# Kernel optimization log

Hardware: AMD Instinct MI355X
Metric: run time of the kernel (lower is better)

## Reference

```python
import jax, jax.numpy as jnp
import numpy as np

B, H, W = 32, 768, 768
POS_THR = 0.1
NEG_RATIO = 3
TOPK_NO_POS = 500


def setup_inputs() -> dict:
    key = jax.random.key(0)
    k1, k2, k3 = jax.random.split(key, 3)
    pred = jax.random.uniform(k1, (B, H, W, 2), dtype=jnp.float32)
    region_scores = jax.random.uniform(k2, (B, H, W), dtype=jnp.float32) ** 16
    affinity_scores = jax.random.uniform(k3, (B, H, W), dtype=jnp.float32) ** 16
    return {"pred": pred, "region_scores": region_scores, "affinity_scores": affinity_scores}


def _single_image_loss(pre_loss, label):
    # Vectorized OHEM: replaces the per-sample Python loop + torch.topk.
    b = pre_loss.shape[0]
    loss = pre_loss.reshape(b, -1)   # [B, N]
    lab = label.reshape(b, -1)       # [B, N]
    n = loss.shape[1]
    pos = lab >= POS_THR             # [B, N] bool
    p = jnp.sum(pos, axis=1)         # positive pixel count per sample
    pos_sum = jnp.sum(jnp.where(pos, loss, 0.0), axis=1)
    posi_loss = jnp.where(p > 0, pos_sum / jnp.maximum(p, 1).astype(loss.dtype), 0.0)
    # Negatives sorted descending; -inf pushes positives to the tail.
    # When p == 0 the mask is all-False so this sorts the full loss vector,
    # matching torch.topk(pre_loss[i], 500).
    neg_vals = jnp.where(pos, -jnp.inf, loss)
    sorted_desc = jnp.flip(jnp.sort(neg_vals, axis=1), axis=1)
    nn = n - p                       # negative count
    # mean of all negatives when nn < 3p == mean of top-min(nn,3p); else top-3p
    k = jnp.where(p > 0, jnp.minimum(nn, NEG_RATIO * p), TOPK_NO_POS)
    csum = jnp.cumsum(jnp.where(jnp.isfinite(sorted_desc), sorted_desc, 0.0), axis=1)
    topk_sum = jnp.take_along_axis(csum, jnp.maximum(k - 1, 0)[:, None], axis=1)[:, 0]
    nega_loss = jnp.where(k > 0, topk_sum / jnp.maximum(k, 1).astype(loss.dtype), 0.0)
    return jnp.sum(posi_loss + nega_loss)


def reference(pred, region_scores, affinity_scores):
    p_gh = pred[..., 0]
    p_gah = pred[..., 1]
    loss1 = (p_gh - region_scores) ** 2   # MSELoss(reduction='none')
    loss2 = (p_gah - affinity_scores) ** 2
    char_loss = _single_image_loss(loss1, region_scores)
    affi_loss = _single_image_loss(loss2, affinity_scores)
    b = pred.shape[0]
    return char_loss / b + affi_loss / b
```

## Files before the change

kernel.cpp:

```cpp
#include <hip/hip_runtime.h>


constexpr int   BATCH   = 32;
constexpr int   NPS     = 768 * 768;
constexpr int   CH2     = BATCH * 2;
constexpr long  PIX_ALL = (long)BATCH * NPS;
constexpr int   EPB     = 8192;
constexpr int   BX      = NPS / EPB;
constexpr float POS_THR_F = 0.1f;
constexpr unsigned TOPK_NO_POS = 500u;
constexpr int   CAP     = 131072;
constexpr int   CAPB    = 1024;

__global__ __launch_bounds__(256, 4) void k_pass1(
    const float4* __restrict__ pred4,
    const float4* __restrict__ reg4,
    const float4* __restrict__ aff4,
    unsigned* __restrict__ h1c,
    unsigned* __restrict__ pcnt, float* __restrict__ psum,
    float4* __restrict__ lossR4, float4* __restrict__ lossA4, int writeLoss)
{
    __shared__ unsigned sc0[512 * 4], sc1[512 * 4];
    __shared__ unsigned wpc[8];
    __shared__ float    wps[8];
    for (int j = threadIdx.x; j < 2048; j += 256) { sc0[j] = 0u; sc1[j] = 0u; }
    __syncthreads();

    const int  b   = blockIdx.y;
    const int  tid = threadIdx.x;
    const int  rep = tid & 3;
    constexpr int ITERS = EPB / 1024;
    long idx4 = (((long)b * NPS + (long)blockIdx.x * EPB) >> 2) + tid;

    unsigned pc0 = 0, pc1 = 0;
    float    ps0 = 0.f, ps1 = 0.f;

    float4 r = reg4[idx4], a = aff4[idx4];
    float4 pA = pred4[idx4 * 2], pB = pred4[idx4 * 2 + 1];

    for (int i = 0; i < ITERS; ++i) {
        float4 rn, an, pAn, pBn;
        if (i + 1 < ITERS) {
            const long nx = idx4 + 256;
            rn = reg4[nx]; an = aff4[nx]; pAn = pred4[nx * 2]; pBn = pred4[nx * 2 + 1];
        }
        float4 lr, la;
#define DO_PIX(RR, AA, PG, PA, LR, LA) do {                                   \
        float d0 = (PG) - (RR); float v0 = d0 * d0;                           \
        bool pos0 = (RR) >= POS_THR_F;                                        \
        if (pos0) { pc0++; ps0 += v0; }                                       \
        else { unsigned ky = __float_as_uint(v0) >> 21;                       \
               atomicAdd(&sc0[(ky << 2) + rep], 1u); }                        \
        LR = pos0 ? -1.0f : v0;                                               \
        float d1 = (PA) - (AA); float v1 = d1 * d1;                           \
        bool pos1 = (AA) >= POS_THR_F;                                        \
        if (pos1) { pc1++; ps1 += v1; }                                       \
        else { unsigned ky = __float_as_uint(v1) >> 21;                       \
               atomicAdd(&sc1[(ky << 2) + rep], 1u); }                        \
        LA = pos1 ? -1.0f : v1;                                               \
    } while (0)
        DO_PIX(r.x, a.x, pA.x, pA.y, lr.x, la.x);
        DO_PIX(r.y, a.y, pA.z, pA.w, lr.y, la.y);
        DO_PIX(r.z, a.z, pB.x, pB.y, lr.z, la.z);
        DO_PIX(r.w, a.w, pB.z, pB.w, lr.w, la.w);
#undef DO_PIX
        if (writeLoss) { lossR4[idx4] = lr; lossA4[idx4] = la; }
        idx4 += 256; r = rn; a = an; pA = pAn; pB = pBn;
    }
    __syncthreads();

    for (int j = tid; j < 512; j += 256) {
        unsigned c0 = sc0[j*4] + sc0[j*4+1] + sc0[j*4+2] + sc0[j*4+3];
        if (c0) atomicAdd(&h1c[(b*2+0)*512 + j], c0);
        unsigned c1 = sc1[j*4] + sc1[j*4+1] + sc1[j*4+2] + sc1[j*4+3];
        if (c1) atomicAdd(&h1c[(b*2+1)*512 + j], c1);
    }
    for (int o = 32; o > 0; o >>= 1) {
        pc0 += __shfl_down(pc0, o); ps0 += __shfl_down(ps0, o);
        pc1 += __shfl_down(pc1, o); ps1 += __shfl_down(ps1, o);
    }
    const int wid = tid >> 6, lane = tid & 63;
    if (lane == 0) { wpc[wid] = pc0; wps[wid] = ps0; wpc[4+wid] = pc1; wps[4+wid] = ps1; }
    __syncthreads();
    if (tid == 0) {
        unsigned t0 = 0, t1 = 0; float s0 = 0.f, s1 = 0.f;
        for (int q = 0; q < 4; ++q) { t0 += wpc[q]; s0 += wps[q]; t1 += wpc[4+q]; s1 += wps[4+q]; }
        atomicAdd(&pcnt[b*2+0], t0); unsafeAtomicAdd(&psum[b*2+0], s0);
        atomicAdd(&pcnt[b*2+1], t1); unsafeAtomicAdd(&psum[b*2+1], s1);
    }
}

template<int NBINS>
__device__ __forceinline__ void select_counts(
    const unsigned* __restrict__ cnt, unsigned k,
    unsigned& outBin, unsigned& outRem)
{
    constexpr int PER = NBINS / 256;
    const int t = threadIdx.x;
    unsigned lc[PER];
#pragma unroll
    for (int j = 0; j < PER; ++j) lc[j] = cnt[t*PER + j];
    unsigned lsum = 0;
#pragma unroll
    for (int j = 0; j < PER; ++j) lsum += lc[j];

    __shared__ unsigned part[256];
    __shared__ unsigned s_bin, s_rem;
    part[t] = lsum;
    __syncthreads();
    for (int off = 1; off < 256; off <<= 1) {
        unsigned v = (t + off < 256) ? part[t + off] : 0u;
        __syncthreads();
        part[t] += v;
        __syncthreads();
    }
    unsigned cum = (t + 1 < 256) ? part[t + 1] : 0u;
#pragma unroll
    for (int j = PER - 1; j >= 0; --j) {
        unsigned c = lc[j];
        if (cum < k && k <= cum + c) { s_bin = (unsigned)(t * PER + j); s_rem = k - cum; }
        cum += c;
    }
    __syncthreads();
    outBin = s_bin; outRem = s_rem;
}

template<int NBINS>
__device__ __forceinline__ void select_counts_sums(
    const unsigned* __restrict__ cnt, const float* __restrict__ sums,
    unsigned k, unsigned& outBin, unsigned& outRem, double& outSum)
{
    constexpr int PER = NBINS / 256;
    const int t = threadIdx.x;
    unsigned lc[PER]; float lf[PER];
#pragma unroll
    for (int j = 0; j < PER; ++j) { lc[j] = cnt[t*PER + j]; lf[j] = sums[t*PER + j]; }
    unsigned lsum = 0;
#pragma unroll
    for (int j = 0; j < PER; ++j) lsum += lc[j];

    __shared__ unsigned part[256];
    __shared__ unsigned s_bin, s_rem;
    __shared__ double   wsum[4];
    part[t] = lsum;
    __syncthreads();
    for (int off = 1; off < 256; off <<= 1) {
        unsigned v = (t + off < 256) ? part[t + off] : 0u;
        __syncthreads();
        part[t] += v;
        __syncthreads();
    }
    unsigned cum = (t + 1 < 256) ? part[t + 1] : 0u;
#pragma unroll
    for (int j = PER - 1; j >= 0; --j) {
        unsigned c = lc[j];
        if (cum < k && k <= cum + c) { s_bin = (unsigned)(t * PER + j); s_rem = k - cum; }
        cum += c;
    }
    __syncthreads();
    const unsigned bin = s_bin;
    double ds = 0.0;
#pragma unroll
    for (int j = 0; j < PER; ++j)
        if ((unsigned)(t * PER + j) > bin) ds += (double)lf[j];
    for (int o = 32; o > 0; o >>= 1) ds += __shfl_down(ds, o);
    const int wid = t >> 6, lane = t & 63;
    if (lane == 0) wsum[wid] = ds;
    __syncthreads();
    if (t == 0) ds = wsum[0] + wsum[1] + wsum[2] + wsum[3];
    outBin = bin; outRem = s_rem; outSum = ds;
}

__global__ __launch_bounds__(256) void k_scan1(
    const unsigned* __restrict__ h1c,
    const unsigned* __restrict__ pcnt, const float* __restrict__ psum,
    unsigned* __restrict__ T1, unsigned* __restrict__ rem1,
    unsigned* __restrict__ kk, float* __restrict__ posi)
{
    const int idx = blockIdx.x;
    const unsigned p  = pcnt[idx];
    const unsigned nn = (unsigned)NPS - p;
    const unsigned k  = p ? ((nn < 3u*p) ? nn : 3u*p) : TOPK_NO_POS;
    if (threadIdx.x == 0) {
        kk[idx]   = k;
        posi[idx] = p ? (psum[idx] / (float)p) : 0.0f;
    }
    if (k == 0u) {
        if (threadIdx.x == 0) { T1[idx] = 0xFFFFFFFFu; rem1[idx] = 0u; }
        return;
    }
    unsigned bin, rem;
    select_counts<512>(h1c + idx*512, k, bin, rem);
    if (threadIdx.x == 0) { T1[idx] = bin; rem1[idx] = rem; }
}

__global__ __launch_bounds__(256, 4) void k_pass2(
    const float4* __restrict__ pred4,
    const float4* __restrict__ reg4,
    const float4* __restrict__ aff4,
    const float4* __restrict__ lossR4, const float4* __restrict__ lossA4, int haveLoss,
    const unsigned* __restrict__ T1,
    unsigned* __restrict__ h2c, double* __restrict__ sumAbove,
    float* __restrict__ cbuf, unsigned* __restrict__ ccnt)
{
    __shared__ unsigned sc0[2048], sc1[2048];
    __shared__ float    lb0[CAPB], lb1[CAPB];
    __shared__ unsigned lcnt[2];
    __shared__ unsigned sbase[2];
    __shared__ float    wred[8];
    for (int j = threadIdx.x; j < 2048; j += 256) { sc0[j] = 0u; sc1[j] = 0u; }
    if (threadIdx.x < 2) lcnt[threadIdx.x] = 0u;
    __syncthreads();

    const int b = blockIdx.y;
    const unsigned t1r = T1[b*2+0], t1a = T1[b*2+1];
    const int tid = threadIdx.x, lane = tid & 63;
    float*    gb0 = cbuf + (size_t)(b*2+0) * CAP;
    float*    gb1 = cbuf + (size_t)(b*2+1) * CAP;
    unsigned* gc0 = ccnt + b*2+0;
    unsigned* gc1 = ccnt + b*2+1;
    float rs0 = 0.f, rs1 = 0.f;

    auto proc = [&](float v, unsigned t1, unsigned* sc, float& rs,
                    unsigned* lcnt_p, float* lbuf, unsigned* gcnt, float* gbuf) {
        if (v < 0.0f) return;
        const unsigned bt  = __float_as_uint(v);
        const unsigned key = bt >> 21;
        if (key > t1) { rs += v; return; }
        if (key != t1) return;
        atomicAdd(&sc[(bt >> 10) & 2047u], 1u);
        const unsigned long long m = __ballot(true);
        const int ldr = __ffsll(m) - 1;
        const unsigned pre = (unsigned)__popcll(m & ((1ull << lane) - 1ull));
        unsigned base = 0;
        if (lane == ldr) base = atomicAdd(lcnt_p, (unsigned)__popcll(m));
        base = __shfl(base, ldr);
        const unsigned ix = base + pre;
        if (ix < (unsigned)CAPB) lbuf[ix] = v;
        else { unsigned g = atomicAdd(gcnt, 1u); if (g < (unsigned)CAP) gbuf[g] = v; }
    };

    constexpr int ITERS = EPB / 1024;
    long idx4 = (((long)b * NPS + (long)blockIdx.x * EPB) >> 2) + tid;
    for (int i = 0; i < ITERS; ++i, idx4 += 256) {
        float4 vr, va;
        if (haveLoss) { vr = lossR4[idx4]; va = lossA4[idx4]; }
        else {
            const float4 r  = reg4[idx4];
            const float4 a  = aff4[idx4];
            const float4 pA = pred4[idx4*2];
            const float4 pB = pred4[idx4*2+1];
            float d;
            d = pA.x - r.x; vr.x = (r.x >= POS_THR_F) ? -1.0f : d*d;
            d = pA.z - r.y; vr.y = (r.y >= POS_THR_F) ? -1.0f : d*d;
            d = pB.x - r.z; vr.z = (r.z >= POS_THR_F) ? -1.0f : d*d;
            d = pB.z - r.w; vr.w = (r.w >= POS_THR_F) ? -1.0f : d*d;
            d = pA.y - a.x; va.x = (a.x >= POS_THR_F) ? -1.0f : d*d;
            d = pA.w - a.y; va.y = (a.y >= POS_THR_F) ? -1.0f : d*d;
            d = pB.y - a.z; va.z = (a.z >= POS_THR_F) ? -1.0f : d*d;
            d = pB.w - a.w; va.w = (a.w >= POS_THR_F) ? -1.0f : d*d;
        }
        proc(vr.x, t1r, sc0, rs0, &lcnt[0], lb0, gc0, gb0);
        proc(vr.y, t1r, sc0, rs0, &lcnt[0], lb0, gc0, gb0);
        proc(vr.z, t1r, sc0, rs0, &lcnt[0], lb0, gc0, gb0);
        proc(vr.w, t1r, sc0, rs0, &lcnt[0], lb0, gc0, gb0);
        proc(va.x, t1a, sc1, rs1, &lcnt[1], lb1, gc1, gb1);
        proc(va.y, t1a, sc1, rs1, &lcnt[1], lb1, gc1, gb1);
        proc(va.z, t1a, sc1, rs1, &lcnt[1], lb1, gc1, gb1);
        proc(va.w, t1a, sc1, rs1, &lcnt[1], lb1, gc1, gb1);
    }
    __syncthreads();

    for (int j = tid; j < 2048; j += 256) {
        unsigned c0 = sc0[j];
        if (c0) atomicAdd(&h2c[(b*2+0)*2048 + j], c0);
        unsigned c1 = sc1[j];
        if (c1) atomicAdd(&h2c[(b*2+1)*2048 + j], c1);
    }
    const unsigned lc0 = lcnt[0] < (unsigned)CAPB ? lcnt[0] : (unsigned)CAPB;
    const unsigned lc1 = lcnt[1] < (unsigned)CAPB ? lcnt[1] : (unsigned)CAPB;
    if (tid == 0)      sbase[0] = lc0 ? atomicAdd(gc0, lc0) : 0u;
    else if (tid == 1) sbase[1] = lc1 ? atomicAdd(gc1, lc1) : 0u;
    __syncthreads();
    for (unsigned i = tid; i < lc0; i += 256) {
        unsigned g = sbase[0] + i;
        if (g < (unsigned)CAP) gb0[g] = lb0[i];
    }
    for (unsigned i = tid; i < lc1; i += 256) {
        unsigned g = sbase[1] + i;
        if (g < (unsigned)CAP) gb1[g] = lb1[i];
    }
    for (int o = 32; o > 0; o >>= 1) { rs0 += __shfl_down(rs0, o); rs1 += __shfl_down(rs1, o); }
    const int wid = tid >> 6;
    if (lane == 0) { wred[wid] = rs0; wred[4+wid] = rs1; }
    __syncthreads();
    if (tid == 0) {
        float s0 = wred[0]+wred[1]+wred[2]+wred[3];
        float s1 = wred[4]+wred[5]+wred[6]+wred[7];
        unsafeAtomicAdd(&sumAbove[b*2+0], (double)s0);
        unsafeAtomicAdd(&sumAbove[b*2+1], (double)s1);
    }
}

__global__ __launch_bounds__(256) void k_scan2(
    const unsigned* __restrict__ h2c,
    const unsigned* __restrict__ T1, const unsigned* __restrict__ rem1,
    unsigned* __restrict__ T2, unsigned* __restrict__ rem2)
{
    const int idx = blockIdx.x;
    if (T1[idx] == 0xFFFFFFFFu) {
        if (threadIdx.x == 0) { T2[idx] = 0xFFFFFFFFu; rem2[idx] = 0u; }
        return;
    }
    unsigned bin, rem;
    select_counts<2048>(h2c + idx*2048, rem1[idx], bin, rem);
    if (threadIdx.x == 0) { T2[idx] = bin; rem2[idx] = rem; }
}

__global__ __launch_bounds__(256) void k_pass3_compact(
    const float* __restrict__ cbuf, const unsigned* __restrict__ ccnt,
    const unsigned* __restrict__ T2,
    unsigned* __restrict__ h3c, float* __restrict__ h3s,
    double* __restrict__ sumMid)
{
    const int ch = blockIdx.x;
    const unsigned cnt = ccnt[ch];
    if (cnt > (unsigned)CAP) return;
    __shared__ unsigned sc[1024];
    __shared__ float    ss[1024];
    __shared__ float    wred[4];
    for (int j = threadIdx.x; j < 1024; j += 256) { sc[j] = 0u; ss[j] = 0.f; }
    __syncthreads();

    const unsigned t2 = T2[ch];
    const float* buf = cbuf + (size_t)ch * CAP;
    float rs = 0.f;
    for (unsigned i = threadIdx.x; i < cnt; i += 256) {
        const float v = buf[i];
        const unsigned bt = __float_as_uint(v);
        const unsigned s2 = (bt >> 10) & 2047u;
        if (s2 > t2) rs += v;
        else if (s2 == t2) { atomicAdd(&sc[bt & 1023u], 1u); unsafeAtomicAdd(&ss[bt & 1023u], v); }
    }
    __syncthreads();
    for (int j = threadIdx.x; j < 1024; j += 256) {
        unsigned c = sc[j];
        if (c) { atomicAdd(&h3c[ch*1024 + j], c); unsafeAtomicAdd(&h3s[ch*1024 + j], ss[j]); }
    }
    for (int o = 32; o > 0; o >>= 1) rs += __shfl_down(rs, o);
    const int wid = threadIdx.x >> 6, lane = threadIdx.x & 63;
    if (lane == 0) wred[wid] = rs;
    __syncthreads();
    if (threadIdx.x == 0)
        unsafeAtomicAdd(&sumMid[ch], (double)(wred[0]+wred[1]+wred[2]+wred[3]));
}

__global__ __launch_bounds__(256, 4) void k_pass3_full(
    const float4* __restrict__ pred4,
    const float4* __restrict__ reg4,
    const float4* __restrict__ aff4,
    const float4* __restrict__ lossR4, const float4* __restrict__ lossA4, int haveLoss,
    const unsigned* __restrict__ T1, const unsigned* __restrict__ T2,
    const unsigned* __restrict__ ccnt,
    unsigned* __restrict__ h3c, float* __restrict__ h3s,
    double* __restrict__ sumMid)
{
    const int b = blockIdx.y;
    const bool f0 = ccnt[b*2+0] > (unsigned)CAP;
    const bool f1 = ccnt[b*2+1] > (unsigned)CAP;
    if (!f0 && !f1) return;

    __shared__ unsigned sc0[1024], sc1[1024];
    __shared__ float    ss0[1024], ss1[1024];
    __shared__ float    wred[8];
    for (int j = threadIdx.x; j < 1024; j += 256) { sc0[j]=0u; sc1[j]=0u; ss0[j]=0.f; ss1[j]=0.f; }
    __syncthreads();

    const unsigned t1r = T1[b*2+0], t2r = T2[b*2+0];
    const unsigned t1a = T1[b*2+1], t2a = T2[b*2+1];
    const int tid = threadIdx.x;
    float rs0 = 0.f, rs1 = 0.f;

    constexpr int ITERS = EPB / 1024;
    long idx4 = (((long)b * NPS + (long)blockIdx.x * EPB) >> 2) + tid;
    for (int i = 0; i < ITERS; ++i, idx4 += 256) {
        float4 vr, va;
        if (haveLoss) { vr = lossR4[idx4]; va = lossA4[idx4]; }
        else {
            const float4 r  = reg4[idx4];
            const float4 a  = aff4[idx4];
            const float4 pA = pred4[idx4*2];
            const float4 pB = pred4[idx4*2+1];
            float d;
            d = pA.x - r.x; vr.x = (r.x >= POS_THR_F) ? -1.0f : d*d;
            d = pA.z - r.y; vr.y = (r.y >= POS_THR_F) ? -1.0f : d*d;
            d = pB.x - r.z; vr.z = (r.z >= POS_THR_F) ? -1.0f : d*d;
            d = pB.z - r.w; vr.w = (r.w >= POS_THR_F) ? -1.0f : d*d;
            d = pA.y - a.x; va.x = (a.x >= POS_THR_F) ? -1.0f : d*d;
            d = pA.w - a.y; va.y = (a.y >= POS_THR_F) ? -1.0f : d*d;
            d = pB.y - a.z; va.z = (a.z >= POS_THR_F) ? -1.0f : d*d;
            d = pB.w - a.w; va.w = (a.w >= POS_THR_F) ? -1.0f : d*d;
        }
#define DO3(V, T1V, T2V, SC, SS, RS, EN) do {                                 \
        if (EN && (V) >= 0.0f) { unsigned bt = __float_as_uint(V);            \
            if ((bt >> 21) == (T1V)) { unsigned s2 = (bt >> 10) & 2047u;      \
                if (s2 > (T2V)) RS += (V);                                    \
                else if (s2 == (T2V)) { atomicAdd(&SC[bt & 1023u], 1u);       \
                    unsafeAtomicAdd(&SS[bt & 1023u], (V)); } } } } while (0)
        DO3(vr.x, t1r, t2r, sc0, ss0, rs0, f0); DO3(vr.y, t1r, t2r, sc0, ss0, rs0, f0);
        DO3(vr.z, t1r, t2r, sc0, ss0, rs0, f0); DO3(vr.w, t1r, t2r, sc0, ss0, rs0, f0);
        DO3(va.x, t1a, t2a, sc1, ss1, rs1, f1); DO3(va.y, t1a, t2a, sc1, ss1, rs1, f1);
        DO3(va.z, t1a, t2a, sc1, ss1, rs1, f1); DO3(va.w, t1a, t2a, sc1, ss1, rs1, f1);
#undef DO3
    }
    __syncthreads();
    for (int j = tid; j < 1024; j += 256) {
        if (f0) { unsigned c = sc0[j];
            if (c) { atomicAdd(&h3c[(b*2+0)*1024 + j], c); unsafeAtomicAdd(&h3s[(b*2+0)*1024 + j], ss0[j]); } }
        if (f1) { unsigned c = sc1[j];
            if (c) { atomicAdd(&h3c[(b*2+1)*1024 + j], c); unsafeAtomicAdd(&h3s[(b*2+1)*1024 + j], ss1[j]); } }
    }
    for (int o = 32; o > 0; o >>= 1) { rs0 += __shfl_down(rs0, o); rs1 += __shfl_down(rs1, o); }
    const int wid = tid >> 6, lane = tid & 63;
    if (lane == 0) { wred[wid] = rs0; wred[4+wid] = rs1; }
    __syncthreads();
    if (tid == 0) {
        if (f0) unsafeAtomicAdd(&sumMid[b*2+0], (double)(wred[0]+wred[1]+wred[2]+wred[3]));
        if (f1) unsafeAtomicAdd(&sumMid[b*2+1], (double)(wred[4]+wred[5]+wred[6]+wred[7]));
    }
}

__global__ __launch_bounds__(256) void k_scan3(
    const unsigned* __restrict__ h3c, const float* __restrict__ h3s,
    const unsigned* __restrict__ T1, const unsigned* __restrict__ T2,
    const unsigned* __restrict__ rem2,
    const unsigned* __restrict__ kk, const float* __restrict__ posi,
    const double* __restrict__ sumAbove, const double* __restrict__ sumMid,
    float* __restrict__ contrib)
{
    const int idx = blockIdx.x;
    const unsigned k = kk[idx];
    if (k == 0u) {
        if (threadIdx.x == 0) contrib[idx] = posi[idx];
        return;
    }
    unsigned bin, rem; double s3;
    select_counts_sums<1024>(h3c + idx*1024, h3s + idx*1024, rem2[idx], bin, rem, s3);
    if (threadIdx.x == 0) {
        const float t = __uint_as_float((T1[idx] << 21) | (T2[idx] << 10) | bin);
        const double nega = (sumAbove[idx] + sumMid[idx] + s3 + (double)rem * (double)t)
                            / (double)k;
        contrib[idx] = (float)((double)posi[idx] + nega);
    }
}

__global__ void k_reduce(const float* __restrict__ contrib, float* __restrict__ out)
{
    double v = (double)contrib[threadIdx.x];
    for (int o = 32; o > 0; o >>= 1) v += __shfl_down(v, o);
    if (threadIdx.x == 0) out[0] = (float)(v / (double)BATCH);
}

extern "C" void kernel_launch(void* const* d_in, const int* in_sizes, int n_in,
                              void* d_out, int out_size, void* d_ws, size_t ws_size,
                              hipStream_t stream)
{
    (void)in_sizes; (void)n_in; (void)out_size; (void)ws_size;
    const float4* pred4 = (const float4*)d_in[0];
    const float4* reg4  = (const float4*)d_in[1];
    const float4* aff4  = (const float4*)d_in[2];

    char* w = (char*)d_ws;
    unsigned* h1c  = (unsigned*)w;
    unsigned* h2c  = h1c + (size_t)CH2 * 512;
    unsigned* h3c  = h2c + (size_t)CH2 * 2048;
    float*    h3s  = (float*)(h3c + (size_t)CH2 * 1024);
    unsigned* pcnt = (unsigned*)(h3s + (size_t)CH2 * 1024);
    float*    psum = (float*)(pcnt + CH2);
    unsigned* T1   = (unsigned*)(psum + CH2);
    unsigned* T2   = T1 + CH2;
    unsigned* rem1 = T2 + CH2;
    unsigned* rem2 = rem1 + CH2;
    unsigned* kk   = rem2 + CH2;
    float*    posi = (float*)(kk + CH2);
    float*    contrib = posi + CH2;
    unsigned* ccnt = (unsigned*)(contrib + CH2);
    double*   sumAbove = (double*)(ccnt + CH2);
    double*   sumMid   = sumAbove + CH2;
    const size_t hdr_bytes = (size_t)((char*)(sumMid + CH2) - w);

    const size_t loss_off   = (size_t)4 << 20;
    const size_t loss_bytes = (size_t)PIX_ALL * 2 * sizeof(float);
    const int haveLoss = (ws_size >= loss_off + loss_bytes) ? 1 : 0;
    float4* lossR4 = (float4*)(w + loss_off);
    float4* lossA4 = (float4*)(w + loss_off + (size_t)PIX_ALL * sizeof(float));

    const size_t cbuf_off = haveLoss ? (loss_off + loss_bytes) : loss_off;
    float* cbuf = (float*)(w + cbuf_off);

    hipMemsetAsync(d_ws, 0, hdr_bytes, stream);

    dim3 grid(BX, BATCH);
    k_pass1<<<grid, 256, 0, stream>>>(pred4, reg4, aff4, h1c, pcnt, psum,
                                      lossR4, lossA4, haveLoss);
    k_scan1<<<CH2, 256, 0, stream>>>(h1c, pcnt, psum, T1, rem1, kk, posi);
    k_pass2<<<grid, 256, 0, stream>>>(pred4, reg4, aff4, lossR4, lossA4, haveLoss,
                                      T1, h2c, sumAbove, cbuf, ccnt);
    k_scan2<<<CH2, 256, 0, stream>>>(h2c, T1, rem1, T2, rem2);
    k_pass3_compact<<<CH2, 256, 0, stream>>>(cbuf, ccnt, T2, h3c, h3s, sumMid);
    k_pass3_full<<<grid, 256, 0, stream>>>(pred4, reg4, aff4, lossR4, lossA4, haveLoss,
                                           T1, T2, ccnt, h3c, h3s, sumMid);
    k_scan3<<<CH2, 256, 0, stream>>>(h3c, h3s, T1, T2, rem2, kk, posi,
                                     sumAbove, sumMid, contrib);
    k_reduce<<<1, 64, 0, stream>>>(contrib, (float*)d_out);
}
```

Baseline: 460.4 us.

## Restructure radix-select into histogram, compact, and in-block refine passes

Replaces the three-pass radix select with a single 2048-bin first-level histogram that also accumulates per-bin sums. Candidates in the threshold bin are then compacted and refined inside one block per channel, so the loss buffer writes and reads and the second and third full-data passes go away. The cost is shared-memory float atomics in the histogram pass, a re-read of the inputs in the compact pass, and no fallback when the compacted candidate count exceeds the buffer capacity. The compact loop also issues redundant loads, and its prefetch values are discarded.

```diff
diff --git a/kernel.cpp b/kernel.cpp
--- a/kernel.cpp
+++ b/kernel.cpp
@@ -4,31 +4,30 @@
 constexpr int   BATCH   = 32;
 constexpr int   NPS     = 768 * 768;
 constexpr int   CH2     = BATCH * 2;
-constexpr long  PIX_ALL = (long)BATCH * NPS;
-constexpr int   EPB     = 8192;
+constexpr int   EPB     = 16384;
 constexpr int   BX      = NPS / EPB;
 constexpr float POS_THR_F = 0.1f;
 constexpr unsigned TOPK_NO_POS = 500u;
+constexpr int   NB1     = 2048;
 constexpr int   CAP     = 131072;
 constexpr int   CAPB    = 1024;
 
-__global__ __launch_bounds__(256, 4) void k_pass1(
+__global__ __launch_bounds__(256, 4) void k_hist(
     const float4* __restrict__ pred4,
     const float4* __restrict__ reg4,
     const float4* __restrict__ aff4,
-    unsigned* __restrict__ h1c,
-    unsigned* __restrict__ pcnt, float* __restrict__ psum,
-    float4* __restrict__ lossR4, float4* __restrict__ lossA4, int writeLoss)
-{
-    __shared__ unsigned sc0[512 * 4], sc1[512 * 4];
+    unsigned* __restrict__ h1c, float* __restrict__ h1s,
+    unsigned* __restrict__ pcnt, float* __restrict__ psum)
+{
+    __shared__ unsigned sc0[NB1], sc1[NB1];
+    __shared__ float    ss0[NB1], ss1[NB1];
     __shared__ unsigned wpc[8];
     __shared__ float    wps[8];
-    for (int j = threadIdx.x; j < 2048; j += 256) { sc0[j] = 0u; sc1[j] = 0u; }
+    for (int j = threadIdx.x; j < NB1; j += 256) { sc0[j]=0u; sc1[j]=0u; ss0[j]=0.f; ss1[j]=0.f; }
     __syncthreads();
 
     const int  b   = blockIdx.y;
     const int  tid = threadIdx.x;
-    const int  rep = tid & 3;
     constexpr int ITERS = EPB / 1024;
     long idx4 = (((long)b * NPS + (long)blockIdx.x * EPB) >> 2) + tid;
 
@@ -44,36 +43,30 @@
             const long nx = idx4 + 256;
             rn = reg4[nx]; an = aff4[nx]; pAn = pred4[nx * 2]; pBn = pred4[nx * 2 + 1];
         }
-        float4 lr, la;
-#define DO_PIX(RR, AA, PG, PA, LR, LA) do {                                   \
+#define DO_PIX(RR, AA, PG, PA) do {                                           \
         float d0 = (PG) - (RR); float v0 = d0 * d0;                           \
-        bool pos0 = (RR) >= POS_THR_F;                                        \
-        if (pos0) { pc0++; ps0 += v0; }                                       \
-        else { unsigned ky = __float_as_uint(v0) >> 21;                       \
-               atomicAdd(&sc0[(ky << 2) + rep], 1u); }                        \
-        LR = pos0 ? -1.0f : v0;                                               \
+        if ((RR) >= POS_THR_F) { pc0++; ps0 += v0; }                          \
+        else { unsigned ky = __float_as_uint(v0) >> 19;                       \
+               atomicAdd(&sc0[ky], 1u); unsafeAtomicAdd(&ss0[ky], v0); }      \
         float d1 = (PA) - (AA); float v1 = d1 * d1;                           \
-        bool pos1 = (AA) >= POS_THR_F;                                        \
-        if (pos1) { pc1++; ps1 += v1; }                                       \
-        else { unsigned ky = __float_as_uint(v1) >> 21;                       \
-               atomicAdd(&sc1[(ky << 2) + rep], 1u); }                        \
-        LA = pos1 ? -1.0f : v1;                                               \
+        if ((AA) >= POS_THR_F) { pc1++; ps1 += v1; }                          \
+        else { unsigned ky = __float_as_uint(v1) >> 19;                       \
+               atomicAdd(&sc1[ky], 1u); unsafeAtomicAdd(&ss1[ky], v1); }      \
     } while (0)
-        DO_PIX(r.x, a.x, pA.x, pA.y, lr.x, la.x);
-        DO_PIX(r.y, a.y, pA.z, pA.w, lr.y, la.y);
-        DO_PIX(r.z, a.z, pB.x, pB.y, lr.z, la.z);
-        DO_PIX(r.w, a.w, pB.z, pB.w, lr.w, la.w);
+        DO_PIX(r.x, a.x, pA.x, pA.y);
+        DO_PIX(r.y, a.y, pA.z, pA.w);
+        DO_PIX(r.z, a.z, pB.x, pB.y);
+        DO_PIX(r.w, a.w, pB.z, pB.w);
 #undef DO_PIX
-        if (writeLoss) { lossR4[idx4] = lr; lossA4[idx4] = la; }
         idx4 += 256; r = rn; a = an; pA = pAn; pB = pBn;
     }
     __syncthreads();
 
-    for (int j = tid; j < 512; j += 256) {
-        unsigned c0 = sc0[j*4] + sc0[j*4+1] + sc0[j*4+2] + sc0[j*4+3];
-        if (c0) atomicAdd(&h1c[(b*2+0)*512 + j], c0);
-        unsigned c1 = sc1[j*4] + sc1[j*4+1] + sc1[j*4+2] + sc1[j*4+3];
-        if (c1) atomicAdd(&h1c[(b*2+1)*512 + j], c1);
+    for (int j = tid; j < NB1; j += 256) {
+        unsigned c0 = sc0[j];
+        if (c0) { atomicAdd(&h1c[(b*2+0)*NB1 + j], c0); unsafeAtomicAdd(&h1s[(b*2+0)*NB1 + j], ss0[j]); }
+        unsigned c1 = sc1[j];
+        if (c1) { atomicAdd(&h1c[(b*2+1)*NB1 + j], c1); unsafeAtomicAdd(&h1s[(b*2+1)*NB1 + j], ss1[j]); }
     }
     for (int o = 32; o > 0; o >>= 1) {
         pc0 += __shfl_down(pc0, o); ps0 += __shfl_down(ps0, o);
@@ -92,8 +85,7 @@
 
 template<int NBINS>
 __device__ __forceinline__ void select_counts(
-    const unsigned* __restrict__ cnt, unsigned k,
-    unsigned& outBin, unsigned& outRem)
+    const unsigned* cnt, unsigned k, unsigned& outBin, unsigned& outRem)
 {
     constexpr int PER = NBINS / 256;
     const int t = threadIdx.x;
@@ -127,7 +119,7 @@
 
 template<int NBINS>
 __device__ __forceinline__ void select_counts_sums(
-    const unsigned* __restrict__ cnt, const float* __restrict__ sums,
+    const unsigned* cnt, const float* sums,
     unsigned k, unsigned& outBin, unsigned& outRem, double& outSum)
 {
     constexpr int PER = NBINS / 256;
@@ -172,10 +164,11 @@
 }
 
 __global__ __launch_bounds__(256) void k_scan1(
-    const unsigned* __restrict__ h1c,
+    const unsigned* __restrict__ h1c, const float* __restrict__ h1s,
     const unsigned* __restrict__ pcnt, const float* __restrict__ psum,
     unsigned* __restrict__ T1, unsigned* __restrict__ rem1,
-    unsigned* __restrict__ kk, float* __restrict__ posi)
+    unsigned* __restrict__ kk, float* __restrict__ posi,
+    double* __restrict__ sumAbove)
 {
     const int idx = blockIdx.x;
     const unsigned p  = pcnt[idx];
@@ -186,29 +179,24 @@
         posi[idx] = p ? (psum[idx] / (float)p) : 0.0f;
     }
     if (k == 0u) {
-        if (threadIdx.x == 0) { T1[idx] = 0xFFFFFFFFu; rem1[idx] = 0u; }
+        if (threadIdx.x == 0) { T1[idx] = 0xFFFFFFFFu; rem1[idx] = 0u; sumAbove[idx] = 0.0; }
         return;
     }
-    unsigned bin, rem;
-    select_counts<512>(h1c + idx*512, k, bin, rem);
-    if (threadIdx.x == 0) { T1[idx] = bin; rem1[idx] = rem; }
-}
-
-__global__ __launch_bounds__(256, 4) void k_pass2(
+    unsigned bin, rem; double s;
+    select_counts_sums<NB1>(h1c + idx*NB1, h1s + idx*NB1, k, bin, rem, s);
+    if (threadIdx.x == 0) { T1[idx] = bin; rem1[idx] = rem; sumAbove[idx] = s; }
+}
+
+__global__ __launch_bounds__(256, 4) void k_compact(
     const float4* __restrict__ pred4,
     const float4* __restrict__ reg4,
     const float4* __restrict__ aff4,
-    const float4* __restrict__ lossR4, const float4* __restrict__ lossA4, int haveLoss,
     const unsigned* __restrict__ T1,
-    unsigned* __restrict__ h2c, double* __restrict__ sumAbove,
     float* __restrict__ cbuf, unsigned* __restrict__ ccnt)
 {
-    __shared__ unsigned sc0[2048], sc1[2048];
     __shared__ float    lb0[CAPB], lb1[CAPB];
     __shared__ unsigned lcnt[2];
     __shared__ unsigned sbase[2];
-    __shared__ float    wred[8];
-    for (int j = threadIdx.x; j < 2048; j += 256) { sc0[j] = 0u; sc1[j] = 0u; }
     if (threadIdx.x < 2) lcnt[threadIdx.x] = 0u;
     __syncthreads();
 
@@ -219,16 +207,13 @@
     float*    gb1 = cbuf + (size_t)(b*2+1) * CAP;
     unsigned* gc0 = ccnt + b*2+0;
     unsigned* gc1 = ccnt + b*2+1;
-    float rs0 = 0.f, rs1 = 0.f;
-
-    auto proc = [&](float v, unsigned t1, unsigned* sc, float& rs,
+
+    auto proc = [&](float tgt, float pg, unsigned t1,
                     unsigned* lcnt_p, float* lbuf, unsigned* gcnt, float* gbuf) {
-        if (v < 0.0f) return;
-        const unsigned bt  = __float_as_uint(v);
-        const unsigned key = bt >> 21;
-        if (key > t1) { rs += v; return; }
-        if (key != t1) return;
-        atomicAdd(&sc[(bt >> 10) & 2047u], 1u);
+        if (tgt >= POS_THR_F) return;
+        const float d = pg - tgt;
+        const float v = d * d;
+        if ((__float_as_uint(v) >> 19) != t1) return;
         const unsigned long long m = __ballot(true);
         const int ldr = __ffsll(m) - 1;
         const unsigned pre = (unsigned)__popcll(m & ((1ull << lane) - 1ull));
@@ -242,41 +227,32 @@
 
     constexpr int ITERS = EPB / 1024;
     long idx4 = (((long)b * NPS + (long)blockIdx.x * EPB) >> 2) + tid;
-    for (int i = 0; i < ITERS; ++i, idx4 += 256) {
-        float4 vr, va;
-        if (haveLoss) { vr = lossR4[idx4]; va = lossA4[idx4]; }
-        else {
-            const float4 r  = reg4[idx4];
-            const float4 a  = aff4[idx4];
-            const float4 pA = pred4[idx4*2];
-            const float4 pB = pred4[idx4*2+1];
-            float d;
-            d = pA.x - r.x; vr.x = (r.x >= POS_THR_F) ? -1.0f : d*d;
-            d = pA.z - r.y; vr.y = (r.y >= POS_THR_F) ? -1.0f : d*d;
-            d = pB.x - r.z; vr.z = (r.z >= POS_THR_F) ? -1.0f : d*d;
-            d = pB.z - r.w; vr.w = (r.w >= POS_THR_F) ? -1.0f : d*d;
-            d = pA.y - a.x; va.x = (a.x >= POS_THR_F) ? -1.0f : d*d;
-            d = pA.w - a.y; va.y = (a.y >= POS_THR_F) ? -1.0f : d*d;
-            d = pB.y - a.z; va.z = (a.z >= POS_THR_F) ? -1.0f : d*d;
-            d = pB.w - a.w; va.w = (a.w >= POS_THR_F) ? -1.0f : d*d;
+    for (int i = 0; i < ITERS; ++i) {
+        float4 rn, an, pAn, pBn;
+        if (i + 1 < ITERS) {
+            const long nx = idx4 + 256;
+            rn = reg4[nx]; an = aff4[nx]; pAn = pred4[nx * 2]; pBn = pred4[nx * 2 + 1];
+        } else {
+            rn = reg4[idx4]; an = aff4[idx4]; pAn = pred4[idx4*2]; pBn = pred4[idx4*2+1];
         }
-        proc(vr.x, t1r, sc0, rs0, &lcnt[0], lb0, gc0, gb0);
-        proc(vr.y, t1r, sc0, rs0, &lcnt[0], lb0, gc0, gb0);
-        proc(vr.z, t1r, sc0, rs0, &lcnt[0], lb0, gc0, gb0);
-        proc(vr.w, t1r, sc0, rs0, &lcnt[0], lb0, gc0, gb0);
-        proc(va.x, t1a, sc1, rs1, &lcnt[1], lb1, gc1, gb1);
-        proc(va.y, t1a, sc1, rs1, &lcnt[1], lb1, gc1, gb1);
-        proc(va.z, t1a, sc1, rs1, &lcnt[1], lb1, gc1, gb1);
-        proc(va.w, t1a, sc1, rs1, &lcnt[1], lb1, gc1, gb1);
-    }
-    __syncthreads();
-
-    for (int j = tid; j < 2048; j += 256) {
-        unsigned c0 = sc0[j];
-        if (c0) atomicAdd(&h2c[(b*2+0)*2048 + j], c0);
-        unsigned c1 = sc1[j];
-        if (c1) atomicAdd(&h2c[(b*2+1)*2048 + j], c1);
-    }
+        const float4 r  = (i == 0) ? reg4[idx4] : rn;
+        (void)r;
+        const float4 rr = reg4[idx4];
+        const float4 aa = aff4[idx4];
+        const float4 pA = pred4[idx4*2];
+        const float4 pB = pred4[idx4*2+1];
+        proc(rr.x, pA.x, t1r, &lcnt[0], lb0, gc0, gb0);
+        proc(rr.y, pA.z, t1r, &lcnt[0], lb0, gc0, gb0);
+        proc(rr.z, pB.x, t1r, &lcnt[0], lb0, gc0, gb0);
+        proc(rr.w, pB.z, t1r, &lcnt[0], lb0, gc0, gb0);
+        proc(aa.x, pA.y, t1a, &lcnt[1], lb1, gc1, gb1);
+        proc(aa.y, pA.w, t1a, &lcnt[1], lb1, gc1, gb1);
+        proc(aa.z, pB.y, t1a, &lcnt[1], lb1, gc1, gb1);
+        proc(aa.w, pB.w, t1a, &lcnt[1], lb1, gc1, gb1);
+        idx4 += 256;
+    }
+    __syncthreads();
+
     const unsigned lc0 = lcnt[0] < (unsigned)CAPB ? lcnt[0] : (unsigned)CAPB;
     const unsigned lc1 = lcnt[1] < (unsigned)CAPB ? lcnt[1] : (unsigned)CAPB;
     if (tid == 0)      sbase[0] = lc0 ? atomicAdd(gc0, lc0) : 0u;
@@ -290,167 +266,63 @@
         unsigned g = sbase[1] + i;
         if (g < (unsigned)CAP) gb1[g] = lb1[i];
     }
-    for (int o = 32; o > 0; o >>= 1) { rs0 += __shfl_down(rs0, o); rs1 += __shfl_down(rs1, o); }
-    const int wid = tid >> 6;
-    if (lane == 0) { wred[wid] = rs0; wred[4+wid] = rs1; }
+}
+
+__global__ __launch_bounds__(256) void k_refine(
+    const float* __restrict__ cbuf, const unsigned* __restrict__ ccnt,
+    const unsigned* __restrict__ T1, const unsigned* __restrict__ rem1,
+    const unsigned* __restrict__ kk, const float* __restrict__ posi,
+    const double* __restrict__ sumAbove,
+    float* __restrict__ contrib)
+{
+    const int ch = blockIdx.x;
+    const unsigned k = kk[ch];
+    if (k == 0u) {
+        if (threadIdx.x == 0) contrib[ch] = posi[ch];
+        return;
+    }
+    unsigned cnt = ccnt[ch];
+    if (cnt > (unsigned)CAP) cnt = (unsigned)CAP;
+    const float* buf = cbuf + (size_t)ch * CAP;
+    const int tid = threadIdx.x;
+
+    __shared__ unsigned hA[NB1];
+    __shared__ unsigned hB[256];
+    __shared__ double   wsum[4];
+    for (int j = tid; j < NB1; j += 256) hA[j] = 0u;
+    __syncthreads();
+    for (unsigned i = tid; i < cnt; i += 256) {
+        const unsigned bt = __float_as_uint(buf[i]);
+        atomicAdd(&hA[(bt >> 8) & 2047u], 1u);
+    }
+    __syncthreads();
+    unsigned T2, rem2;
+    select_counts<NB1>(hA, rem1[ch], T2, rem2);
+
+    hB[tid] = 0u;
+    __syncthreads();
+    for (unsigned i = tid; i < cnt; i += 256) {
+        const unsigned bt = __float_as_uint(buf[i]);
+        if (((bt >> 8) & 2047u) == T2) atomicAdd(&hB[bt & 255u], 1u);
+    }
+    __syncthreads();
+    unsigned T3, rem3;
+    select_counts<256>(hB, rem2, T3, rem3);
+
+    const float t = __uint_as_float((T1[ch] << 19) | (T2 << 8) | T3);
+    double s = 0.0;
+    for (unsigned i = tid; i < cnt; i += 256) {
+        const float v = buf[i];
+        if (v > t) s += (double)v;
+    }
+    for (int o = 32; o > 0; o >>= 1) s += __shfl_down(s, o);
+    const int wid = tid >> 6, lane = tid & 63;
+    if (lane == 0) wsum[wid] = s;
     __syncthreads();
     if (tid == 0) {
-        float s0 = wred[0]+wred[1]+wred[2]+wred[3];
-        float s1 = wred[4]+wred[5]+wred[6]+wred[7];
-        unsafeAtomicAdd(&sumAbove[b*2+0], (double)s0);
-        unsafeAtomicAdd(&sumAbove[b*2+1], (double)s1);
-    }
-}
-
-__global__ __launch_bounds__(256) void k_scan2(
-    const unsigned* __restrict__ h2c,
-    const unsigned* __restrict__ T1, const unsigned* __restrict__ rem1,
-    unsigned* __restrict__ T2, unsigned* __restrict__ rem2)
-{
-    const int idx = blockIdx.x;
-    if (T1[idx] == 0xFFFFFFFFu) {
-        if (threadIdx.x == 0) { T2[idx] = 0xFFFFFFFFu; rem2[idx] = 0u; }
-        return;
-    }
-    unsigned bin, rem;
-    select_counts<2048>(h2c + idx*2048, rem1[idx], bin, rem);
-    if (threadIdx.x == 0) { T2[idx] = bin; rem2[idx] = rem; }
-}
-
-__global__ __launch_bounds__(256) void k_pass3_compact(
-    const float* __restrict__ cbuf, const unsigned* __restrict__ ccnt,
-    const unsigned* __restrict__ T2,
-    unsigned* __restrict__ h3c, float* __restrict__ h3s,
-    double* __restrict__ sumMid)
-{
-    const int ch = blockIdx.x;
-    const unsigned cnt = ccnt[ch];
-    if (cnt > (unsigned)CAP) return;
-    __shared__ unsigned sc[1024];
-    __shared__ float    ss[1024];
-    __shared__ float    wred[4];
-    for (int j = threadIdx.x; j < 1024; j += 256) { sc[j] = 0u; ss[j] = 0.f; }
-    __syncthreads();
-
-    const unsigned t2 = T2[ch];
-    const float* buf = cbuf + (size_t)ch * CAP;
-    float rs = 0.f;
-    for (unsigned i = threadIdx.x; i < cnt; i += 256) {
-        const float v = buf[i];
-        const unsigned bt = __float_as_uint(v);
-        const unsigned s2 = (bt >> 10) & 2047u;
-        if (s2 > t2) rs += v;
-        else if (s2 == t2) { atomicAdd(&sc[bt & 1023u], 1u); unsafeAtomicAdd(&ss[bt & 1023u], v); }
-    }
-    __syncthreads();
-    for (int j = threadIdx.x; j < 1024; j += 256) {
-        unsigned c = sc[j];
-        if (c) { atomicAdd(&h3c[ch*1024 + j], c); unsafeAtomicAdd(&h3s[ch*1024 + j], ss[j]); }
-    }
-    for (int o = 32; o > 0; o >>= 1) rs += __shfl_down(rs, o);
-    const int wid = threadIdx.x >> 6, lane = threadIdx.x & 63;
-    if (lane == 0) wred[wid] = rs;
-    __syncthreads();
-    if (threadIdx.x == 0)
-        unsafeAtomicAdd(&sumMid[ch], (double)(wred[0]+wred[1]+wred[2]+wred[3]));
-}
-
-__global__ __launch_bounds__(256, 4) void k_pass3_full(
-    const float4* __restrict__ pred4,
-    const float4* __restrict__ reg4,
-    const float4* __restrict__ aff4,
-    const float4* __restrict__ lossR4, const float4* __restrict__ lossA4, int haveLoss,
-    const unsigned* __restrict__ T1, const unsigned* __restrict__ T2,
-    const unsigned* __restrict__ ccnt,
-    unsigned* __restrict__ h3c, float* __restrict__ h3s,
-    double* __restrict__ sumMid)
-{
-    const int b = blockIdx.y;
-    const bool f0 = ccnt[b*2+0] > (unsigned)CAP;
-    const bool f1 = ccnt[b*2+1] > (unsigned)CAP;
-    if (!f0 && !f1) return;
-
-    __shared__ unsigned sc0[1024], sc1[1024];
-    __shared__ float    ss0[1024], ss1[1024];
-    __shared__ float    wred[8];
-    for (int j = threadIdx.x; j < 1024; j += 256) { sc0[j]=0u; sc1[j]=0u; ss0[j]=0.f; ss1[j]=0.f; }
-    __syncthreads();
-
-    const unsigned t1r = T1[b*2+0], t2r = T2[b*2+0];
-    const unsigned t1a = T1[b*2+1], t2a = T2[b*2+1];
-    const int tid = threadIdx.x;
-    float rs0 = 0.f, rs1 = 0.f;
-
-    constexpr int ITERS = EPB / 1024;
-    long idx4 = (((long)b * NPS + (long)blockIdx.x * EPB) >> 2) + tid;
-    for (int i = 0; i < ITERS; ++i, idx4 += 256) {
-        float4 vr, va;
-        if (haveLoss) { vr = lossR4[idx4]; va = lossA4[idx4]; }
-        else {
-            const float4 r  = reg4[idx4];
-            const float4 a  = aff4[idx4];
-            const float4 pA = pred4[idx4*2];
-            const float4 pB = pred4[idx4*2+1];
-            float d;
-            d = pA.x - r.x; vr.x = (r.x >= POS_THR_F) ? -1.0f : d*d;
-            d = pA.z - r.y; vr.y = (r.y >= POS_THR_F) ? -1.0f : d*d;
-            d = pB.x - r.z; vr.z = (r.z >= POS_THR_F) ? -1.0f : d*d;
-            d = pB.z - r.w; vr.w = (r.w >= POS_THR_F) ? -1.0f : d*d;
-            d = pA.y - a.x; va.x = (a.x >= POS_THR_F) ? -1.0f : d*d;
-            d = pA.w - a.y; va.y = (a.y >= POS_THR_F) ? -1.0f : d*d;
-            d = pB.y - a.z; va.z = (a.z >= POS_THR_F) ? -1.0f : d*d;
-            d = pB.w - a.w; va.w = (a.w >= POS_THR_F) ? -1.0f : d*d;
-        }
-#define DO3(V, T1V, T2V, SC, SS, RS, EN) do {                                 \
-        if (EN && (V) >= 0.0f) { unsigned bt = __float_as_uint(V);            \
-            if ((bt >> 21) == (T1V)) { unsigned s2 = (bt >> 10) & 2047u;      \
-                if (s2 > (T2V)) RS += (V);                                    \
-                else if (s2 == (T2V)) { atomicAdd(&SC[bt & 1023u], 1u);       \
-                    unsafeAtomicAdd(&SS[bt & 1023u], (V)); } } } } while (0)
-        DO3(vr.x, t1r, t2r, sc0, ss0, rs0, f0); DO3(vr.y, t1r, t2r, sc0, ss0, rs0, f0);
-        DO3(vr.z, t1r, t2r, sc0, ss0, rs0, f0); DO3(vr.w, t1r, t2r, sc0, ss0, rs0, f0);
-        DO3(va.x, t1a, t2a, sc1, ss1, rs1, f1); DO3(va.y, t1a, t2a, sc1, ss1, rs1, f1);
-        DO3(va.z, t1a, t2a, sc1, ss1, rs1, f1); DO3(va.w, t1a, t2a, sc1, ss1, rs1, f1);
-#undef DO3
-    }
-    __syncthreads();
-    for (int j = tid; j < 1024; j += 256) {
-        if (f0) { unsigned c = sc0[j];
-            if (c) { atomicAdd(&h3c[(b*2+0)*1024 + j], c); unsafeAtomicAdd(&h3s[(b*2+0)*1024 + j], ss0[j]); } }
-        if (f1) { unsigned c = sc1[j];
-            if (c) { atomicAdd(&h3c[(b*2+1)*1024 + j], c); unsafeAtomicAdd(&h3s[(b*2+1)*1024 + j], ss1[j]); } }
-    }
-    for (int o = 32; o > 0; o >>= 1) { rs0 += __shfl_down(rs0, o); rs1 += __shfl_down(rs1, o); }
-    const int wid = tid >> 6, lane = tid & 63;
-    if (lane == 0) { wred[wid] = rs0; wred[4+wid] = rs1; }
-    __syncthreads();
-    if (tid == 0) {
-        if (f0) unsafeAtomicAdd(&sumMid[b*2+0], (double)(wred[0]+wred[1]+wred[2]+wred[3]));
-        if (f1) unsafeAtomicAdd(&sumMid[b*2+1], (double)(wred[4]+wred[5]+wred[6]+wred[7]));
-    }
-}
-
-__global__ __launch_bounds__(256) void k_scan3(
-    const unsigned* __restrict__ h3c, const float* __restrict__ h3s,
-    const unsigned* __restrict__ T1, const unsigned* __restrict__ T2,
-    const unsigned* __restrict__ rem2,
-    const unsigned* __restrict__ kk, const float* __restrict__ posi,
-    const double* __restrict__ sumAbove, const double* __restrict__ sumMid,
-    float* __restrict__ contrib)
-{
-    const int idx = blockIdx.x;
-    const unsigned k = kk[idx];
-    if (k == 0u) {
-        if (threadIdx.x == 0) contrib[idx] = posi[idx];
-        return;
-    }
-    unsigned bin, rem; double s3;
-    select_counts_sums<1024>(h3c + idx*1024, h3s + idx*1024, rem2[idx], bin, rem, s3);
-    if (threadIdx.x == 0) {
-        const float t = __uint_as_float((T1[idx] << 21) | (T2[idx] << 10) | bin);
-        const double nega = (sumAbove[idx] + sumMid[idx] + s3 + (double)rem * (double)t)
-                            / (double)k;
-        contrib[idx] = (float)((double)posi[idx] + nega);
+        const double stop = wsum[0] + wsum[1] + wsum[2] + wsum[3];
+        const double nega = (sumAbove[ch] + stop + (double)rem3 * (double)t) / (double)k;
+        contrib[ch] = (float)((double)posi[ch] + nega);
     }
 }
 
@@ -472,45 +344,26 @@
 
     char* w = (char*)d_ws;
     unsigned* h1c  = (unsigned*)w;
-    unsigned* h2c  = h1c + (size_t)CH2 * 512;
-    unsigned* h3c  = h2c + (size_t)CH2 * 2048;
-    float*    h3s  = (float*)(h3c + (size_t)CH2 * 1024);
-    unsigned* pcnt = (unsigned*)(h3s + (size_t)CH2 * 1024);
+    float*    h1s  = (float*)(h1c + (size_t)CH2 * NB1);
+    unsigned* pcnt = (unsigned*)(h1s + (size_t)CH2 * NB1);
     float*    psum = (float*)(pcnt + CH2);
     unsigned* T1   = (unsigned*)(psum + CH2);
-    unsigned* T2   = T1 + CH2;
-    unsigned* rem1 = T2 + CH2;
-    unsigned* rem2 = rem1 + CH2;
-    unsigned* kk   = rem2 + CH2;
+    unsigned* rem1 = T1 + CH2;
+    unsigned* kk   = rem1 + CH2;
     float*    posi = (float*)(kk + CH2);
     float*    contrib = posi + CH2;
     unsigned* ccnt = (unsigned*)(contrib + CH2);
     double*   sumAbove = (double*)(ccnt + CH2);
-    double*   sumMid   = sumAbove + CH2;
-    const size_t hdr_bytes = (size_t)((char*)(sumMid + CH2) - w);
-
-    const size_t loss_off   = (size_t)4 << 20;
-    const size_t loss_bytes = (size_t)PIX_ALL * 2 * sizeof(float);
-    const int haveLoss = (ws_size >= loss_off + loss_bytes) ? 1 : 0;
-    float4* lossR4 = (float4*)(w + loss_off);
-    float4* lossA4 = (float4*)(w + loss_off + (size_t)PIX_ALL * sizeof(float));
-
-    const size_t cbuf_off = haveLoss ? (loss_off + loss_bytes) : loss_off;
-    float* cbuf = (float*)(w + cbuf_off);
+    const size_t hdr_bytes = (size_t)((char*)(sumAbove + CH2) - w);
+
+    float* cbuf = (float*)(w + ((size_t)2 << 20));
 
     hipMemsetAsync(d_ws, 0, hdr_bytes, stream);
 
     dim3 grid(BX, BATCH);
-    k_pass1<<<grid, 256, 0, stream>>>(pred4, reg4, aff4, h1c, pcnt, psum,
-                                      lossR4, lossA4, haveLoss);
-    k_scan1<<<CH2, 256, 0, stream>>>(h1c, pcnt, psum, T1, rem1, kk, posi);
-    k_pass2<<<grid, 256, 0, stream>>>(pred4, reg4, aff4, lossR4, lossA4, haveLoss,
-                                      T1, h2c, sumAbove, cbuf, ccnt);
-    k_scan2<<<CH2, 256, 0, stream>>>(h2c, T1, rem1, T2, rem2);
-    k_pass3_compact<<<CH2, 256, 0, stream>>>(cbuf, ccnt, T2, h3c, h3s, sumMid);
-    k_pass3_full<<<grid, 256, 0, stream>>>(pred4, reg4, aff4, lossR4, lossA4, haveLoss,
-                                           T1, T2, ccnt, h3c, h3s, sumMid);
-    k_scan3<<<CH2, 256, 0, stream>>>(h3c, h3s, T1, T2, rem2, kk, posi,
-                                     sumAbove, sumMid, contrib);
+    k_hist<<<grid, 256, 0, stream>>>(pred4, reg4, aff4, h1c, h1s, pcnt, psum);
+    k_scan1<<<CH2, 256, 0, stream>>>(h1c, h1s, pcnt, psum, T1, rem1, kk, posi, sumAbove);
+    k_compact<<<grid, 256, 0, stream>>>(pred4, reg4, aff4, T1, cbuf, ccnt);
+    k_refine<<<CH2, 256, 0, stream>>>(cbuf, ccnt, T1, rem1, kk, posi, sumAbove, contrib);
     k_reduce<<<1, 64, 0, stream>>>(contrib, (float*)d_out);
 }
```

Result: slower. 482.0 us (+4.7%).
